# Kernel tuning notes

Hardware: AMD Instinct MI355X
Metric: run time of the kernel (lower is better)

## Reference

```python
import jax, jax.numpy as jnp
import numpy as np

B, H, T, D = 2, 16, 2048, 64
BASE_WINDOW = 256
FULL = 999999


def _make_window_sizes(num_heads=H, base_window=BASE_WINDOW):
    ws = []
    for h in range(num_heads):
        if h < num_heads // 4:
            ws.append(base_window)
        elif h < num_heads // 2:
            ws.append(base_window * 2)
        elif h < 3 * num_heads // 4:
            ws.append(base_window * 4)
        else:
            ws.append(FULL)
    return jnp.asarray(ws, dtype=jnp.int32)


def setup_inputs() -> dict:
    key = jax.random.key(0)
    kq, kk, kv = jax.random.split(key, 3)
    Q = jax.random.normal(kq, (B, H, T, D), dtype=jnp.float32)
    K = jax.random.normal(kk, (B, H, T, D), dtype=jnp.float32)
    V = jax.random.normal(kv, (B, H, T, D), dtype=jnp.float32)
    return {"Q": Q, "K": K, "V": V, "window_sizes": _make_window_sizes()}


def reference(Q, K, V, window_sizes):
    b, h, t, d = Q.shape
    scale = 1.0 / np.sqrt(d).astype(np.float32)
    idx = jnp.arange(t, dtype=jnp.int32)
    diff = idx[:, None] - idx[None, :]  # [T, T], q_idx - kv_idx
    # causal & |q-k| <= w  ==  0 <= diff <= w  (per head)
    mask = (diff >= 0) & (diff[None, :, :] <= window_sizes[:, None, None])  # [H, T, T]
    scores = jnp.einsum('bhqd,bhkd->bhqk', Q, K) * scale  # [B, H, T, T]
    scores = jnp.where(mask[None], scores, -jnp.inf)
    attn = jax.nn.softmax(scores, axis=-1)
    return jnp.einsum('bhqk,bhkd->bhqd', attn, V)
```

## Files before the change

kernel.cpp:

```cpp
#include <hip/hip_runtime.h>
#include <hip/hip_bf16.h>


constexpr int Bc = 2, Hc = 16, Tc = 2048, Dc = 64;
constexpr int BQ = 64;
constexpr int BK = 64;
constexpr int N_ITEMS = Bc * Hc * (Tc / BQ);
constexpr float QSCALE = 0.125f * 1.44269504088896340736f;
constexpr float CMAX = 16.0f;

constexpr size_t KB_OFF = 256;
constexpr size_t VB_OFF = 256 + (size_t)Bc * Hc * Tc * Dc * 2;
constexpr int HEADE = Tc * Dc;

constexpr int KOFF = 0;
constexpr int VOFF = 8192;
constexpr int POFF = 16384;
constexpr int IBOFF = 24576;

typedef __attribute__((ext_vector_type(8))) short short8;
typedef __attribute__((ext_vector_type(4))) float float4v;

#if defined(__has_builtin)
#if __has_builtin(__builtin_amdgcn_exp2f)
#define EXP2 __builtin_amdgcn_exp2f
#endif
#endif
#ifndef EXP2
#define EXP2 exp2f
#endif

__device__ inline unsigned f2bf_u(float f) {
    union { float f; unsigned u; } v; v.f = f;
    return (v.u + 0x7fffu + ((v.u >> 16) & 1u)) >> 16;
}

__device__ inline short8 pack8(const float* t) {
    short8 r;
#pragma unroll
    for (int j = 0; j < 8; j++) r[j] = (short)f2bf_u(t[j]);
    return r;
}

__device__ inline unsigned pk_bf16(float a, float b) {
    __hip_bfloat162 h = __float22bfloat162_rn(make_float2(a, b));
    union { __hip_bfloat162 h; unsigned u; } v; v.h = h;
    return v.u;
}

__device__ inline int swz(int row, int col8) {
    return row * 64 + (col8 ^ ((row & 7) << 3));
}

__global__ __launch_bounds__(256)
void preconv_kernel(const float* __restrict__ K, const float* __restrict__ V,
                    unsigned short* __restrict__ Kb, unsigned short* __restrict__ Vtb) {
    const int blk = blockIdx.x;
    const int tid = threadIdx.x;
    if (blk < 2048) {
        const int base = blk * 2048 + tid * 8;
        float4v a = *(const float4v*)(K + base);
        float4v b = *(const float4v*)(K + base + 4);
        float t[8] = {a[0], a[1], a[2], a[3], b[0], b[1], b[2], b[3]};
        *(short8*)(Kb + base) = pack8(t);
    } else {
        __shared__ float tile[64][65];
        const int blk2 = blk - 2048;
        const int bh = blk2 >> 5;
        const int t0 = (blk2 & 31) * 64;
        const float* src = V + (size_t)bh * HEADE + (size_t)t0 * Dc;
#pragma unroll
        for (int i = 0; i < 4; i++) {
            const int r = (tid >> 4) + i * 16;
            const int d4 = (tid & 15) * 4;
            float4v v4 = *(const float4v*)(src + r * Dc + d4);
            tile[r][d4] = v4[0]; tile[r][d4 + 1] = v4[1];
            tile[r][d4 + 2] = v4[2]; tile[r][d4 + 3] = v4[3];
        }
        __syncthreads();
        unsigned short* dst = Vtb + (size_t)bh * HEADE + t0;
#pragma unroll
        for (int i = 0; i < 2; i++) {
            const int d = (tid >> 3) + 32 * i;
            const int c = tid & 7;
            float t[8];
#pragma unroll
            for (int j = 0; j < 8; j++) t[j] = tile[c * 8 + j][d];
            *(short8*)(dst + (size_t)d * Tc + c * 8) = pack8(t);
        }
    }
}

__global__ __launch_bounds__(512, 4)
void dswa_kernel(const float* __restrict__ Q,
                 const unsigned short* __restrict__ Kb,
                 const unsigned short* __restrict__ Vtb,
                 const int* __restrict__ wsz,
                 float* __restrict__ O, unsigned* __restrict__ counter) {
    __shared__ __align__(16) unsigned short LDS[24576 + 8];

    const int tid  = threadIdx.x;
    const int g    = tid >> 8;
    const int ltid = tid & 255;
    const int wave = tid >> 6;
    const int wv   = wave & 3;
    const int lane = tid & 63;
    const int quad = lane >> 4;
    const int l16  = lane & 15;
    const int sw8  = (l16 & 7) << 3;

    unsigned short* Kl = &LDS[KOFF + g * 4096];
    unsigned short* Vt = &LDS[VOFF + g * 4096];
    unsigned short* Pl = &LDS[POFF + wave * 1024];
    int* ib = (int*)&LDS[IBOFF];

    const int srow = ltid >> 3;
    const int scol = (ltid & 7) * 8;

    for (;;) {
        if (tid == 0) *ib = (int)atomicAdd(counter, 1u);
        __syncthreads();
        const int idx = *ib;
        if (idx >= N_ITEMS) break;

        const int b  = idx & 1;
        const int qt = 31 - ((idx >> 1) & 31);
        const int h  = 15 - (idx >> 6);
        const int q0 = qt * BQ;
        const int win = wsz[h];

        const size_t headoff = (size_t)(b * Hc + h) * HEADE;
        const float* Qp = Q + headoff;
        const unsigned short* Kbh = Kb + headoff;
        const unsigned short* Vbh = Vtb + headoff;
        float* Op = O + headoff;

        short8 qf[2];
        {
            const int qrow = q0 + wv * 16 + l16;
#pragma unroll
            for (int c = 0; c < 2; c++) {
                const float* src = Qp + (size_t)qrow * Dc + c * 32 + quad * 8;
                float4v a = *(const float4v*)src;
                float4v d4 = *(const float4v*)(src + 4);
                float t[8] = {a[0]*QSCALE, a[1]*QSCALE, a[2]*QSCALE, a[3]*QSCALE,
                              d4[0]*QSCALE, d4[1]*QSCALE, d4[2]*QSCALE, d4[3]*QSCALE};
                qf[c] = pack8(t);
            }
        }

        float4v acc[4];
#pragma unroll
        for (int nb = 0; nb < 4; nb++) acc[nb] = (float4v){0.f, 0.f, 0.f, 0.f};
        float lp = 0.0f;

        const int kv_lo = (max(0, q0 - win)) & ~(BK - 1);
        const int n_tiles = (q0 + BQ - kv_lo) >> 6;
        const int IT = (n_tiles + 1) >> 1;

        const int rw0 = q0 + wv * 16;
        const int rg_rel0 = rw0 + l16 - quad * 4;

        short8 kr0, kr1, vr0, vr1;
        if (g < n_tiles) {
            const int kv0 = kv_lo + g * BK;
            kr0 = *(const short8*)(Kbh + (size_t)(kv0 + srow) * Dc + scol);
            kr1 = *(const short8*)(Kbh + (size_t)(kv0 + srow + 32) * Dc + scol);
            vr0 = *(const short8*)(Vbh + (size_t)srow * Tc + kv0 + scol);
            vr1 = *(const short8*)(Vbh + (size_t)(srow + 32) * Tc + kv0 + scol);
        }

        for (int t = 0; t < IT; ++t) {
            const int ti = g + 2 * t;
            const bool act = ti < n_tiles;
            const int kv0 = kv_lo + ti * BK;

            __syncthreads();

            if (act) {
                *(short8*)&Kl[swz(srow, scol)] = kr0;
                *(short8*)&Kl[swz(srow + 32, scol)] = kr1;
                *(short8*)&Vt[swz(srow, scol)] = vr0;
                *(short8*)&Vt[swz(srow + 32, scol)] = vr1;
            }
            __syncthreads();

            const int tn = ti + 2;
            if (tn < n_tiles) {
                const int kvn = kv_lo + tn * BK;
                kr0 = *(const short8*)(Kbh + (size_t)(kvn + srow) * Dc + scol);
                kr1 = *(const short8*)(Kbh + (size_t)(kvn + srow + 32) * Dc + scol);
                vr0 = *(const short8*)(Vbh + (size_t)srow * Tc + kvn + scol);
                vr1 = *(const short8*)(Vbh + (size_t)(srow + 32) * Tc + kvn + scol);
            }

            if (act) {
                float4v sT[4];
#pragma unroll
                for (int mb = 0; mb < 4; mb++) {
                    float4v c = {-CMAX, -CMAX, -CMAX, -CMAX};
#pragma unroll
                    for (int ch = 0; ch < 2; ch++) {
                        short8 kf = *(short8*)&Kl[(mb * 16 + l16) * 64 +
                                                  ((ch * 32 + quad * 8) ^ sw8)];
                        c = __builtin_amdgcn_mfma_f32_16x16x32_bf16(kf, qf[ch], c, 0, 0, 0);
                    }
                    sT[mb] = c;
                }

                const bool interior = (rw0 >= kv0 + 63) && (rw0 + 15 - kv0 <= win);
                if (!interior) {
                    const int dbase = rg_rel0 - kv0;
#pragma unroll
                    for (int mb = 0; mb < 4; mb++)
#pragma unroll
                        for (int r = 0; r < 4; r++) {
                            const unsigned diff = (unsigned)(dbase - mb * 16 - r);
                            sT[mb][r] = (diff <= (unsigned)win) ? sT[mb][r] : -3.0e38f;
                        }
                }

#pragma unroll
                for (int mb = 0; mb < 4; mb++) {
                    float p0 = EXP2(sT[mb][0]);
                    float p1 = EXP2(sT[mb][1]);
                    float p2 = EXP2(sT[mb][2]);
                    float p3 = EXP2(sT[mb][3]);
                    lp += (p0 + p1) + (p2 + p3);
                    unsigned* dst = (unsigned*)&Pl[l16 * 64 +
                                                   ((mb * 16 + quad * 4) ^ sw8)];
                    dst[0] = pk_bf16(p0, p1);
                    dst[1] = pk_bf16(p2, p3);
                }

                __asm__ volatile("" ::: "memory");
                short8 pf[2];
#pragma unroll
                for (int ch = 0; ch < 2; ch++)
                    pf[ch] = *(short8*)&Pl[l16 * 64 + ((ch * 32 + quad * 8) ^ sw8)];

#pragma unroll
                for (int nb = 0; nb < 4; nb++) {
#pragma unroll
                    for (int ch = 0; ch < 2; ch++) {
                        short8 vf = *(short8*)&Vt[(nb * 16 + l16) * 64 +
                                                  ((ch * 32 + quad * 8) ^ sw8)];
                        acc[nb] = __builtin_amdgcn_mfma_f32_16x16x32_bf16(pf[ch], vf, acc[nb], 0, 0, 0);
                    }
                }
            }
        }

        lp += __shfl_xor(lp, 16);
        lp += __shfl_xor(lp, 32);

        __syncthreads();
        float* fl = (float*)LDS;
        if (g == 1) {
            if (quad == 0) fl[(wv * 16 + l16) * 66 + 64] = lp;
#pragma unroll
            for (int r = 0; r < 4; r++) {
                const int row = wv * 16 + quad * 4 + r;
#pragma unroll
                for (int nb = 0; nb < 4; nb++)
                    fl[row * 66 + nb * 16 + l16] = acc[nb][r];
            }
        }
        __syncthreads();
        if (g == 0) {
#pragma unroll
            for (int r = 0; r < 4; r++) {
                const int row = wv * 16 + quad * 4 + r;
                const float l0 = __shfl(lp, quad * 4 + r);
                const float lt = l0 + fl[row * 66 + 64];
                const float inv = 1.0f / lt;
                float* dst = Op + (size_t)(q0 + row) * Dc;
#pragma unroll
                for (int nb = 0; nb < 4; nb++)
                    dst[nb * 16 + l16] = (acc[nb][r] + fl[row * 66 + nb * 16 + l16]) * inv;
            }
        }
    }
}

extern "C" void kernel_launch(void* const* d_in, const int* in_sizes, int n_in,
                              void* d_out, int out_size, void* d_ws, size_t ws_size,
                              hipStream_t stream) {
    (void)in_sizes; (void)n_in; (void)ws_size; (void)out_size;
    const float* Q = (const float*)d_in[0];
    const float* K = (const float*)d_in[1];
    const float* V = (const float*)d_in[2];
    const int* wsz = (const int*)d_in[3];
    float* Out = (float*)d_out;

    unsigned* counter = (unsigned*)d_ws;
    unsigned short* Kb  = (unsigned short*)((char*)d_ws + KB_OFF);
    unsigned short* Vtb = (unsigned short*)((char*)d_ws + VB_OFF);

    hipMemsetAsync(counter, 0, sizeof(unsigned), stream);
    preconv_kernel<<<dim3(3072), dim3(256), 0, stream>>>(K, V, Kb, Vtb);
    dswa_kernel<<<dim3(768), dim3(512), 0, stream>>>(Q, Kb, Vtb, wsz, Out, counter);
}
```

Measured before the change: 128.7 us.

## Halve block to 4 waves with 32 query rows each, direct global-to-LDS DMA

Each wave now handles two 16-row query slices, sharing each K fragment read across two MFMAs, and blocks shrink to 256 threads with more blocks launched. K/V tiles are loaded with global_load_lds straight into swizzled LDS instead of through register staging, and the workgroup waits for these loads before the barrier. This gives up the previous prefetch of the next tile, which exposes load latency each iteration, and the slot used to broadcast the work index now overlaps the P scratch area.

After: 141.6 us. 1.1x slower.

```diff
diff --git a/kernel.cpp b/kernel.cpp
--- a/kernel.cpp
+++ b/kernel.cpp
@@ -16,7 +16,6 @@
 constexpr int KOFF = 0;
 constexpr int VOFF = 8192;
 constexpr int POFF = 16384;
-constexpr int IBOFF = 24576;
 
 typedef __attribute__((ext_vector_type(8))) short short8;
 typedef __attribute__((ext_vector_type(4))) float float4v;
@@ -48,8 +47,10 @@
     return v.u;
 }
 
-__device__ inline int swz(int row, int col8) {
-    return row * 64 + (col8 ^ ((row & 7) << 3));
+__device__ inline void dma16(const unsigned short* g, unsigned short* l) {
+    __builtin_amdgcn_global_load_lds(
+        (const __attribute__((address_space(1))) unsigned int*)g,
+        (__attribute__((address_space(3))) unsigned int*)l, 16, 0, 0);
 }
 
 __global__ __launch_bounds__(256)
@@ -91,19 +92,18 @@
     }
 }
 
-__global__ __launch_bounds__(512, 4)
+__global__ __launch_bounds__(256, 4)
 void dswa_kernel(const float* __restrict__ Q,
                  const unsigned short* __restrict__ Kb,
                  const unsigned short* __restrict__ Vtb,
                  const int* __restrict__ wsz,
                  float* __restrict__ O, unsigned* __restrict__ counter) {
-    __shared__ __align__(16) unsigned short LDS[24576 + 8];
+    __shared__ __align__(16) unsigned short LDS[20480];
 
     const int tid  = threadIdx.x;
-    const int g    = tid >> 8;
-    const int ltid = tid & 255;
     const int wave = tid >> 6;
-    const int wv   = wave & 3;
+    const int g    = wave >> 1;
+    const int wq   = wave & 1;
     const int lane = tid & 63;
     const int quad = lane >> 4;
     const int l16  = lane & 15;
@@ -112,10 +112,10 @@
     unsigned short* Kl = &LDS[KOFF + g * 4096];
     unsigned short* Vt = &LDS[VOFF + g * 4096];
     unsigned short* Pl = &LDS[POFF + wave * 1024];
-    int* ib = (int*)&LDS[IBOFF];
-
-    const int srow = ltid >> 3;
-    const int scol = (ltid & 7) * 8;
+    int* ib = (int*)&LDS[POFF];
+
+    const int lrow = lane >> 3;
+    const int lcol = ((lane & 7) * 8) ^ ((lrow & 7) << 3);
 
     for (;;) {
         if (tid == 0) *ib = (int)atomicAdd(counter, 1u);
@@ -135,9 +135,10 @@
         const unsigned short* Vbh = Vtb + headoff;
         float* Op = O + headoff;
 
-        short8 qf[2];
-        {
-            const int qrow = q0 + wv * 16 + l16;
+        short8 qf[2][2];
+#pragma unroll
+        for (int s = 0; s < 2; s++) {
+            const int qrow = q0 + wq * 32 + s * 16 + l16;
 #pragma unroll
             for (int c = 0; c < 2; c++) {
                 const float* src = Qp + (size_t)qrow * Dc + c * 32 + quad * 8;
@@ -145,30 +146,24 @@
                 float4v d4 = *(const float4v*)(src + 4);
                 float t[8] = {a[0]*QSCALE, a[1]*QSCALE, a[2]*QSCALE, a[3]*QSCALE,
                               d4[0]*QSCALE, d4[1]*QSCALE, d4[2]*QSCALE, d4[3]*QSCALE};
-                qf[c] = pack8(t);
-            }
-        }
-
-        float4v acc[4];
-#pragma unroll
-        for (int nb = 0; nb < 4; nb++) acc[nb] = (float4v){0.f, 0.f, 0.f, 0.f};
-        float lp = 0.0f;
+                qf[s][c] = pack8(t);
+            }
+        }
+
+        float4v acc[2][4];
+#pragma unroll
+        for (int s = 0; s < 2; s++)
+#pragma unroll
+            for (int nb = 0; nb < 4; nb++) acc[s][nb] = (float4v){0.f, 0.f, 0.f, 0.f};
+        float lp0 = 0.0f, lp1 = 0.0f;
 
         const int kv_lo = (max(0, q0 - win)) & ~(BK - 1);
         const int n_tiles = (q0 + BQ - kv_lo) >> 6;
         const int IT = (n_tiles + 1) >> 1;
 
-        const int rw0 = q0 + wv * 16;
-        const int rg_rel0 = rw0 + l16 - quad * 4;
-
-        short8 kr0, kr1, vr0, vr1;
-        if (g < n_tiles) {
-            const int kv0 = kv_lo + g * BK;
-            kr0 = *(const short8*)(Kbh + (size_t)(kv0 + srow) * Dc + scol);
-            kr1 = *(const short8*)(Kbh + (size_t)(kv0 + srow + 32) * Dc + scol);
-            vr0 = *(const short8*)(Vbh + (size_t)srow * Tc + kv0 + scol);
-            vr1 = *(const short8*)(Vbh + (size_t)(srow + 32) * Tc + kv0 + scol);
-        }
+        const int kv0g = kv_lo + g * BK;
+        const unsigned short* kgp = Kbh + (size_t)(kv0g + wq * 32 + lrow) * 64 + lcol;
+        const unsigned short* vgp = Vbh + (size_t)(wq * 32 + lrow) * Tc + kv0g + lcol;
 
         for (int t = 0; t < IT; ++t) {
             const int ti = g + 2 * t;
@@ -178,66 +173,94 @@
             __syncthreads();
 
             if (act) {
-                *(short8*)&Kl[swz(srow, scol)] = kr0;
-                *(short8*)&Kl[swz(srow + 32, scol)] = kr1;
-                *(short8*)&Vt[swz(srow, scol)] = vr0;
-                *(short8*)&Vt[swz(srow + 32, scol)] = vr1;
-            }
+#pragma unroll
+                for (int j = 0; j < 4; j++)
+                    dma16(kgp + j * 512, &Kl[wq * 2048 + j * 512]);
+#pragma unroll
+                for (int j = 0; j < 4; j++)
+                    dma16(vgp + (size_t)j * 8 * Tc, &Vt[wq * 2048 + j * 512]);
+            }
+            __asm__ volatile("" ::: "memory");
+            __builtin_amdgcn_s_waitcnt(0x0f70);
+            __asm__ volatile("" ::: "memory");
             __syncthreads();
 
-            const int tn = ti + 2;
-            if (tn < n_tiles) {
-                const int kvn = kv_lo + tn * BK;
-                kr0 = *(const short8*)(Kbh + (size_t)(kvn + srow) * Dc + scol);
-                kr1 = *(const short8*)(Kbh + (size_t)(kvn + srow + 32) * Dc + scol);
-                vr0 = *(const short8*)(Vbh + (size_t)srow * Tc + kvn + scol);
-                vr1 = *(const short8*)(Vbh + (size_t)(srow + 32) * Tc + kvn + scol);
-            }
-
             if (act) {
-                float4v sT[4];
+                float4v sT0[4], sT1[4];
 #pragma unroll
                 for (int mb = 0; mb < 4; mb++) {
-                    float4v c = {-CMAX, -CMAX, -CMAX, -CMAX};
+                    float4v c0 = {-CMAX, -CMAX, -CMAX, -CMAX};
+                    float4v c1 = {-CMAX, -CMAX, -CMAX, -CMAX};
 #pragma unroll
                     for (int ch = 0; ch < 2; ch++) {
                         short8 kf = *(short8*)&Kl[(mb * 16 + l16) * 64 +
                                                   ((ch * 32 + quad * 8) ^ sw8)];
-                        c = __builtin_amdgcn_mfma_f32_16x16x32_bf16(kf, qf[ch], c, 0, 0, 0);
-                    }
-                    sT[mb] = c;
-                }
-
-                const bool interior = (rw0 >= kv0 + 63) && (rw0 + 15 - kv0 <= win);
-                if (!interior) {
-                    const int dbase = rg_rel0 - kv0;
-#pragma unroll
-                    for (int mb = 0; mb < 4; mb++)
-#pragma unroll
-                        for (int r = 0; r < 4; r++) {
-                            const unsigned diff = (unsigned)(dbase - mb * 16 - r);
-                            sT[mb][r] = (diff <= (unsigned)win) ? sT[mb][r] : -3.0e38f;
-                        }
-                }
-
-#pragma unroll
-                for (int mb = 0; mb < 4; mb++) {
-                    float p0 = EXP2(sT[mb][0]);
-                    float p1 = EXP2(sT[mb][1]);
-                    float p2 = EXP2(sT[mb][2]);
-                    float p3 = EXP2(sT[mb][3]);
-                    lp += (p0 + p1) + (p2 + p3);
-                    unsigned* dst = (unsigned*)&Pl[l16 * 64 +
-                                                   ((mb * 16 + quad * 4) ^ sw8)];
-                    dst[0] = pk_bf16(p0, p1);
-                    dst[1] = pk_bf16(p2, p3);
-                }
-
-                __asm__ volatile("" ::: "memory");
-                short8 pf[2];
-#pragma unroll
-                for (int ch = 0; ch < 2; ch++)
-                    pf[ch] = *(short8*)&Pl[l16 * 64 + ((ch * 32 + quad * 8) ^ sw8)];
+                        c0 = __builtin_amdgcn_mfma_f32_16x16x32_bf16(kf, qf[0][ch], c0, 0, 0, 0);
+                        c1 = __builtin_amdgcn_mfma_f32_16x16x32_bf16(kf, qf[1][ch], c1, 0, 0, 0);
+                    }
+                    sT0[mb] = c0; sT1[mb] = c1;
+                }
+
+                short8 pf0[2], pf1[2];
+                {
+                    const int rs = q0 + wq * 32;
+                    const bool interior = (rs >= kv0 + 63) && (rs + 15 - kv0 <= win);
+                    if (!interior) {
+                        const int dbase = rs + l16 - kv0 - quad * 4;
+#pragma unroll
+                        for (int mb = 0; mb < 4; mb++)
+#pragma unroll
+                            for (int r = 0; r < 4; r++) {
+                                const unsigned diff = (unsigned)(dbase - mb * 16 - r);
+                                sT0[mb][r] = (diff <= (unsigned)win) ? sT0[mb][r] : -3.0e38f;
+                            }
+                    }
+#pragma unroll
+                    for (int mb = 0; mb < 4; mb++) {
+                        float p0 = EXP2(sT0[mb][0]);
+                        float p1 = EXP2(sT0[mb][1]);
+                        float p2 = EXP2(sT0[mb][2]);
+                        float p3 = EXP2(sT0[mb][3]);
+                        lp0 += (p0 + p1) + (p2 + p3);
+                        unsigned* dst = (unsigned*)&Pl[l16 * 64 + ((mb * 16 + quad * 4) ^ sw8)];
+                        dst[0] = pk_bf16(p0, p1);
+                        dst[1] = pk_bf16(p2, p3);
+                    }
+                    __asm__ volatile("" ::: "memory");
+#pragma unroll
+                    for (int ch = 0; ch < 2; ch++)
+                        pf0[ch] = *(short8*)&Pl[l16 * 64 + ((ch * 32 + quad * 8) ^ sw8)];
+                }
+                {
+                    const int rs = q0 + wq * 32 + 16;
+                    const bool interior = (rs >= kv0 + 63) && (rs + 15 - kv0 <= win);
+                    if (!interior) {
+                        const int dbase = rs + l16 - kv0 - quad * 4;
+#pragma unroll
+                        for (int mb = 0; mb < 4; mb++)
+#pragma unroll
+                            for (int r = 0; r < 4; r++) {
+                                const unsigned diff = (unsigned)(dbase - mb * 16 - r);
+                                sT1[mb][r] = (diff <= (unsigned)win) ? sT1[mb][r] : -3.0e38f;
+                            }
+                    }
+                    __asm__ volatile("" ::: "memory");
+#pragma unroll
+                    for (int mb = 0; mb < 4; mb++) {
+                        float p0 = EXP2(sT1[mb][0]);
+                        float p1 = EXP2(sT1[mb][1]);
+                        float p2 = EXP2(sT1[mb][2]);
+                        float p3 = EXP2(sT1[mb][3]);
+                        lp1 += (p0 + p1) + (p2 + p3);
+                        unsigned* dst = (unsigned*)&Pl[l16 * 64 + ((mb * 16 + quad * 4) ^ sw8)];
+                        dst[0] = pk_bf16(p0, p1);
+                        dst[1] = pk_bf16(p2, p3);
+                    }
+                    __asm__ volatile("" ::: "memory");
+#pragma unroll
+                    for (int ch = 0; ch < 2; ch++)
+                        pf1[ch] = *(short8*)&Pl[l16 * 64 + ((ch * 32 + quad * 8) ^ sw8)];
+                }
 
 #pragma unroll
                 for (int nb = 0; nb < 4; nb++) {
@@ -245,39 +268,49 @@
                     for (int ch = 0; ch < 2; ch++) {
                         short8 vf = *(short8*)&Vt[(nb * 16 + l16) * 64 +
                                                   ((ch * 32 + quad * 8) ^ sw8)];
-                        acc[nb] = __builtin_amdgcn_mfma_f32_16x16x32_bf16(pf[ch], vf, acc[nb], 0, 0, 0);
-                    }
-                }
-            }
-        }
-
-        lp += __shfl_xor(lp, 16);
-        lp += __shfl_xor(lp, 32);
+                        acc[0][nb] = __builtin_amdgcn_mfma_f32_16x16x32_bf16(pf0[ch], vf, acc[0][nb], 0, 0, 0);
+                        acc[1][nb] = __builtin_amdgcn_mfma_f32_16x16x32_bf16(pf1[ch], vf, acc[1][nb], 0, 0, 0);
+                    }
+                }
+            }
+            kgp += 128 * 64;
+            vgp += 128;
+        }
+
+        lp0 += __shfl_xor(lp0, 16); lp0 += __shfl_xor(lp0, 32);
+        lp1 += __shfl_xor(lp1, 16); lp1 += __shfl_xor(lp1, 32);
 
         __syncthreads();
         float* fl = (float*)LDS;
         if (g == 1) {
-            if (quad == 0) fl[(wv * 16 + l16) * 66 + 64] = lp;
-#pragma unroll
-            for (int r = 0; r < 4; r++) {
-                const int row = wv * 16 + quad * 4 + r;
-#pragma unroll
-                for (int nb = 0; nb < 4; nb++)
-                    fl[row * 66 + nb * 16 + l16] = acc[nb][r];
+#pragma unroll
+            for (int s = 0; s < 2; s++) {
+                if (quad == 0) fl[(wq * 32 + s * 16 + l16) * 66 + 64] = (s ? lp1 : lp0);
+#pragma unroll
+                for (int r = 0; r < 4; r++) {
+                    const int row = wq * 32 + s * 16 + quad * 4 + r;
+#pragma unroll
+                    for (int nb = 0; nb < 4; nb++)
+                        fl[row * 66 + nb * 16 + l16] = acc[s][nb][r];
+                }
             }
         }
         __syncthreads();
         if (g == 0) {
 #pragma unroll
-            for (int r = 0; r < 4; r++) {
-                const int row = wv * 16 + quad * 4 + r;
-                const float l0 = __shfl(lp, quad * 4 + r);
-                const float lt = l0 + fl[row * 66 + 64];
-                const float inv = 1.0f / lt;
-                float* dst = Op + (size_t)(q0 + row) * Dc;
-#pragma unroll
-                for (int nb = 0; nb < 4; nb++)
-                    dst[nb * 16 + l16] = (acc[nb][r] + fl[row * 66 + nb * 16 + l16]) * inv;
+            for (int s = 0; s < 2; s++) {
+                const float lps = s ? lp1 : lp0;
+#pragma unroll
+                for (int r = 0; r < 4; r++) {
+                    const int row = wq * 32 + s * 16 + quad * 4 + r;
+                    const float l0 = __shfl(lps, quad * 4 + r);
+                    const float lt = l0 + fl[row * 66 + 64];
+                    const float inv = 1.0f / lt;
+                    float* dst = Op + (size_t)(q0 + row) * Dc;
+#pragma unroll
+                    for (int nb = 0; nb < 4; nb++)
+                        dst[nb * 16 + l16] = (acc[s][nb][r] + fl[row * 66 + nb * 16 + l16]) * inv;
+                }
             }
         }
     }
@@ -299,5 +332,5 @@
 
     hipMemsetAsync(counter, 0, sizeof(unsigned), stream);
     preconv_kernel<<<dim3(3072), dim3(256), 0, stream>>>(K, V, Kb, Vtb);
-    dswa_kernel<<<dim3(768), dim3(512), 0, stream>>>(Q, Kb, Vtb, wsz, Out, counter);
-}
+    dswa_kernel<<<dim3(1024), dim3(256), 0, stream>>>(Q, Kb, Vtb, wsz, Out, counter);
+}
```
